# Optimization experiments

Hardware: AMD Instinct MI355X
Metric: run time of the kernel (lower is better)

Reference implementation:

```python
import jax, jax.numpy as jnp
import numpy as np

ALPHA = 0.2
BN_EPS = 1e-5
NEG = -9e15


def make_quaternion_mul(kernel):
    # kernel: [in/4, out]; split columns into quaternion components
    dim = kernel.shape[1] // 4
    r, i, j, k = jnp.split(kernel, 4, axis=1)
    r2 = jnp.concatenate([r, -i, -j, -k], axis=0)
    i2 = jnp.concatenate([i, r, -k, j], axis=0)
    j2 = jnp.concatenate([j, k, r, -i], axis=0)
    k2 = jnp.concatenate([k, -j, i, r], axis=0)
    return jnp.concatenate([r2, i2, j2, k2], axis=1)  # [in, out]


def setup_inputs() -> dict:
    key = jax.random.key(0)
    k1, k2, k3, k4 = jax.random.split(key, 4)
    N, IN, OUT = 8192, 512, 128
    inp = jax.random.normal(k1, (N, IN), dtype=jnp.float32)
    adj = jax.random.randint(k2, (N, N), 0, 2, dtype=jnp.int32)
    # xavier-like init for params
    W = jax.random.normal(k3, (IN // 4, OUT), dtype=jnp.float32) * (1.0 / np.sqrt(IN // 4))
    a = jax.random.normal(k4, (2 * OUT, 1), dtype=jnp.float32) * (1.0 / np.sqrt(2 * OUT))
    bn_gamma = jnp.ones((OUT,), dtype=jnp.float32)
    bn_beta = jnp.zeros((OUT,), dtype=jnp.float32)
    return {"input": inp, "adj": adj, "W": W, "a": a, "bn_gamma": bn_gamma, "bn_beta": bn_beta}


def reference(input, adj, W, a, bn_gamma, bn_beta):
    out_features = W.shape[1]
    hamilton = make_quaternion_mul(W)           # [in, out]
    h = input @ hamilton                        # [N, out]
    # a_input[i,j] = concat(h_i, h_j); a_input @ a decomposes as
    # (h @ a1)_i + (h @ a2)_j with a1 = a[:out], a2 = a[out:]
    a1 = a[:out_features, 0]                    # [out]
    a2 = a[out_features:, 0]                    # [out]
    s1 = h @ a1                                 # [N]
    s2 = h @ a2                                 # [N]
    e = s1[:, None] + s2[None, :]               # [N, N]
    e = jnp.where(e > 0, e, ALPHA * e)          # leaky_relu
    attention = jnp.where(adj > 0, e, NEG)
    attention = jax.nn.softmax(attention, axis=1)
    # dropout is identity in inference
    h_prime = attention @ h                     # [N, out]
    # BatchNorm1d (training-mode batch statistics, biased variance)
    mean = jnp.mean(h_prime, axis=0)
    var = jnp.var(h_prime, axis=0)
    h_prime = (h_prime - mean) / jnp.sqrt(var + BN_EPS) * bn_gamma + bn_beta
    # concat=True -> ELU
    return jax.nn.elu(h_prime)
```

## Files before the change

### kernel.cpp

```cpp
#include <hip/hip_runtime.h>
#include <hip/hip_bf16.h>
#include <math.h>

#define N_NODES 8192
#define IN_F    512
#define OUT_F   128
#define LRELU_A 0.2f
#define EPS_BN  1e-5f
#define MSH     40.0f
#define NSPLIT  8
#define JSPAN   (N_NODES / NSPLIT)
#define TILE_I  64
#define ISTR    520

typedef unsigned short u16;
typedef unsigned int   u32;
typedef unsigned long long u64;
typedef __attribute__((ext_vector_type(8))) short  short8;
typedef __attribute__((ext_vector_type(4))) float  floatx4;

__device__ __forceinline__ u16 f2bf_rtn(float x) {
    u32 u = __float_as_uint(x);
    return (u16)((u + 0x7fffu + ((u >> 16) & 1u)) >> 16);
}

__global__ __launch_bounds__(256) void k_hamT(const float* __restrict__ W, u16* __restrict__ hamF,
                                              float* __restrict__ s1, float* __restrict__ s2,
                                              float* __restrict__ cs, float* __restrict__ cq) {
    const int idx = blockIdx.x * 256 + threadIdx.x;
    if (idx < N_NODES) { s1[idx] = 0.f; s2[idx] = 0.f; }
    if (idx < OUT_F)   { cs[idx] = 0.f; cq[idx] = 0.f; }
    const int c = idx >> 9, k = idx & 511;
    const int b = c >> 5, cc = c & 31, kp = k >> 7, kq = k & 127;
    const u32 NEGMASK = 0x284Eu;
    const float sg = ((NEGMASK >> (b * 4 + kp)) & 1u) ? -1.f : 1.f;
    const int kappa = k >> 5, q = (k >> 3) & 3, e = k & 7;
    hamF[((kappa * 4 + q) * 128 + c) * 8 + e] = f2bf_rtn(sg * W[kq * 128 + (b ^ kp) * 32 + cc]);
}

__global__ __launch_bounds__(256) void k_h(const float* __restrict__ inp, const u16* __restrict__ hamF,
                                           const float* __restrict__ a,
                                           u16* __restrict__ hT, float* __restrict__ s1, float* __restrict__ s2) {
    __shared__ u16 inA[16 * ISTR];
    __shared__ float red[4][128][20];
    const int t = threadIdx.x;
    const int lane = t & 63, wid = t >> 6;
    const int quad = lane >> 4, n = lane & 15;
    const int i0 = blockIdx.x * 16;
    const int kb = wid * 128;

#pragma unroll
    for (int u = 0; u < 8; ++u) {
        float4 v = *(const float4*)&inp[(size_t)i0 * IN_F + u * 1024 + t * 4];
        const int r = u * 2 + (t >> 7);
        const int col = (t & 127) * 4;
        u64 pk = (u64)f2bf_rtn(v.x) | ((u64)f2bf_rtn(v.y) << 16)
               | ((u64)f2bf_rtn(v.z) << 32) | ((u64)f2bf_rtn(v.w) << 48);
        *(u64*)&inA[r * ISTR + col] = pk;
    }
    __syncthreads();

    floatx4 acc[8];
#pragma unroll
    for (int ct = 0; ct < 8; ++ct) acc[ct] = (floatx4){0.f, 0.f, 0.f, 0.f};

#pragma unroll
    for (int ks = 0; ks < 4; ++ks) {
        short8 fa = *(const short8*)&inA[n * ISTR + kb + ks * 32 + quad * 8];
#pragma unroll
        for (int ct = 0; ct < 8; ++ct) {
            short8 fb = *(const short8*)&hamF[((wid * 4 + ks) * 4 + quad) * 1024 + (ct * 16 + n) * 8];
            acc[ct] = __builtin_amdgcn_mfma_f32_16x16x32_bf16(fa, fb, acc[ct], 0, 0, 0);
        }
    }

    {
        float p1[4] = {0.f, 0.f, 0.f, 0.f}, p2[4] = {0.f, 0.f, 0.f, 0.f};
#pragma unroll
        for (int ct = 0; ct < 8; ++ct) {
            const int c = ct * 16 + n;
            const float a1v = a[c], a2v = a[OUT_F + c];
#pragma unroll
            for (int r = 0; r < 4; ++r) { p1[r] += acc[ct][r] * a1v; p2[r] += acc[ct][r] * a2v; }
        }
#pragma unroll
        for (int m = 1; m < 16; m <<= 1) {
#pragma unroll
            for (int r = 0; r < 4; ++r) {
                p1[r] += __shfl_xor(p1[r], m, 64);
                p2[r] += __shfl_xor(p2[r], m, 64);
            }
        }
        if (n == 0) {
#pragma unroll
            for (int r = 0; r < 4; ++r) {
                atomicAdd(&s1[i0 + quad * 4 + r], p1[r]);
                atomicAdd(&s2[i0 + quad * 4 + r], p2[r]);
            }
        }
    }

#pragma unroll
    for (int ct = 0; ct < 8; ++ct)
        *(float4*)&red[wid][ct * 16 + n][quad * 4] = *(float4*)&acc[ct];
    __syncthreads();

    {
        const int c = t >> 1, ih = (t & 1) * 8;
        float v[8];
#pragma unroll
        for (int e = 0; e < 8; ++e)
            v[e] = red[0][c][ih + e] + red[1][c][ih + e] + red[2][c][ih + e] + red[3][c][ih + e];
        uint4 pk;
        pk.x = (u32)f2bf_rtn(v[0]) | ((u32)f2bf_rtn(v[1]) << 16);
        pk.y = (u32)f2bf_rtn(v[2]) | ((u32)f2bf_rtn(v[3]) << 16);
        pk.z = (u32)f2bf_rtn(v[4]) | ((u32)f2bf_rtn(v[5]) << 16);
        pk.w = (u32)f2bf_rtn(v[6]) | ((u32)f2bf_rtn(v[7]) << 16);
        *(uint4*)&hT[(size_t)c * N_NODES + i0 + ih] = pk;
    }
}

__global__ __launch_bounds__(256, 4) void k_att(const int* __restrict__ adj, const u16* __restrict__ hT,
                                                const float* __restrict__ s1, const float* __restrict__ s2,
                                                float* __restrict__ Opart, float* __restrict__ Lpart) {
    __shared__ u16 hs[2][128 * 64];
    __shared__ float s2s[JSPAN];
    const int t = threadIdx.x;
    const int lane = t & 63, wid = t >> 6;
    const int quad = lane >> 4, n = lane & 15;
    const int i0 = blockIdx.x * TILE_I;
    const int jbase = blockIdx.y * JSPAN;
    const int i_lane = i0 + wid * 16 + n;
    const float s1v = s1[i_lane];
    const int scr = t >> 3, scj = (t & 7) * 8;

    *(float4*)&s2s[t * 4] = *(const float4*)&s2[jbase + t * 4];

    u32 M[4][8];
#pragma unroll
    for (int g = 0; g < 4; ++g)
#pragma unroll
        for (int w = 0; w < 8; ++w) M[g][w] = 0u;
    {
        const size_t rowbase = (size_t)(i0 + wid * 16);
#pragma unroll 4
        for (int rr = 0; rr < 16; ++rr) {
            const int* ap = adj + (rowbase + rr) * N_NODES + jbase + lane * 4;
            uint4 v[4];
#pragma unroll
            for (int g = 0; g < 4; ++g) v[g] = *(const uint4*)(ap + g * 256);
            const bool kp = (n == rr);
#pragma unroll
            for (int g = 0; g < 4; ++g) {
                u64 c0 = __ballot((int)v[g].x > 0);
                u64 c1 = __ballot((int)v[g].y > 0);
                u64 c2 = __ballot((int)v[g].z > 0);
                u64 c3 = __ballot((int)v[g].w > 0);
                if (kp) {
                    M[g][0] = (u32)c0; M[g][1] = (u32)(c0 >> 32);
                    M[g][2] = (u32)c1; M[g][3] = (u32)(c1 >> 32);
                    M[g][4] = (u32)c2; M[g][5] = (u32)(c2 >> 32);
                    M[g][6] = (u32)c3; M[g][7] = (u32)(c3 >> 32);
                }
            }
        }
    }

#pragma unroll
    for (int ps = 0; ps < 4; ++ps) {
        const int cr = ps * 32 + scr;
        uint4 v = *(const uint4*)&hT[(size_t)cr * N_NODES + jbase + scj];
        *(uint4*)&hs[0][cr * 64 + (scj ^ ((cr & 7) * 8))] = v;
    }
    __syncthreads();

    floatx4 acc[8];
#pragma unroll
    for (int ct = 0; ct < 8; ct++) acc[ct] = (floatx4){0.f, 0.f, 0.f, 0.f};
    float Lacc = 0.f;

#pragma unroll
    for (int g = 0; g < 4; ++g) {
#pragma unroll
        for (int chi = 0; chi < 4; ++chi) {
            const int ch = g * 4 + chi;
            const int cur = ch & 1;
            const bool more = (ch + 1 < 16);
            uint4 H[4];
            if (more) {
#pragma unroll
                for (int ps = 0; ps < 4; ++ps) {
                    const int cr = ps * 32 + scr;
                    H[ps] = *(const uint4*)&hT[(size_t)cr * N_NODES + jbase + (ch + 1) * 64 + scj];
                }
            }
            short8 fa[2];
#pragma unroll
            for (int ks = 0; ks < 2; ++ks) {
                const int jl = ch * 64 + ks * 32 + quad * 8;
                float4 sa = *(const float4*)&s2s[jl];
                float4 sb = *(const float4*)&s2s[jl + 4];
                const float sv[8] = {sa.x, sa.y, sa.z, sa.w, sb.x, sb.y, sb.z, sb.w};
                union { u32 u[4]; short8 s; } cv;
#pragma unroll
                for (int jh = 0; jh < 4; ++jh) {
                    float w2[2];
#pragma unroll
                    for (int e = 0; e < 2; ++e) {
                        const int jj = jh * 2 + e;
                        const u32 word = M[g][(jj & 3) * 2 + (chi >> 1)];
                        const int sh = (chi & 1) * 16 + ks * 8 + quad * 2 + (jj >> 2);
                        const u32 mbit = (word >> sh) & 1u;
                        float sc = s1v + sv[jj];
                        sc = fmaxf(sc, LRELU_A * sc);
                        float w = mbit ? __expf(sc - MSH) : 0.f;
                        Lacc += w;
                        w2[e] = w;
                    }
                    cv.u[jh] = (u32)f2bf_rtn(w2[0]) | ((u32)f2bf_rtn(w2[1]) << 16);
                }
                fa[ks] = cv.s;
            }
#pragma unroll
            for (int ct = 0; ct < 8; ++ct) {
                const int rb = ct * 16 + n;
                const int sw = (rb & 7) * 8;
                short8 fb0 = *(const short8*)&hs[cur][rb * 64 + ((quad * 8) ^ sw)];
                short8 fb1 = *(const short8*)&hs[cur][rb * 64 + ((32 + quad * 8) ^ sw)];
                acc[ct] = __builtin_amdgcn_mfma_f32_16x16x32_bf16(fa[0], fb0, acc[ct], 0, 0, 0);
                acc[ct] = __builtin_amdgcn_mfma_f32_16x16x32_bf16(fa[1], fb1, acc[ct], 0, 0, 0);
            }
            if (more) {
#pragma unroll
                for (int ps = 0; ps < 4; ++ps) {
                    const int cr = ps * 32 + scr;
                    *(uint4*)&hs[cur ^ 1][cr * 64 + (scj ^ ((cr & 7) * 8))] = H[ps];
                }
            }
            __syncthreads();
        }
    }

    Lacc += __shfl_xor(Lacc, 16, 64);
    Lacc += __shfl_xor(Lacc, 32, 64);
    if (lane < 16)
        Lpart[(size_t)blockIdx.y * N_NODES + i_lane] = Lacc;

    const size_t obase = (size_t)blockIdx.y * N_NODES * OUT_F;
#pragma unroll
    for (int ct = 0; ct < 8; ++ct) {
#pragma unroll
        for (int r = 0; r < 4; ++r) {
            const int i = i0 + wid * 16 + quad * 4 + r;
            Opart[obase + (size_t)i * OUT_F + ct * 16 + n] = acc[ct][r];
        }
    }
}

__global__ __launch_bounds__(256) void k_comb(const float* __restrict__ Opart, const float* __restrict__ Lpart,
                                              float* __restrict__ hp, float* __restrict__ cs, float* __restrict__ cq) {
    const int t = threadIdx.x;
    const int c = t & 127, half = t >> 7;
    const int ibase = blockIdx.x * 64;
    float sv = 0.f, sq = 0.f;
    for (int k = 0; k < 32; k++) {
        const int i = ibase + half + (k << 1);
        float o = 0.f, L = 0.f;
#pragma unroll
        for (int s = 0; s < NSPLIT; s++) {
            o += Opart[((size_t)s * N_NODES + i) * OUT_F + c];
            L += Lpart[(size_t)s * N_NODES + i];
        }
        float v = L > 0.f ? o / L : 0.f;
        hp[(size_t)i * OUT_F + c] = v;
        sv += v; sq += v * v;
    }
    __shared__ float red[256];
    red[t] = sv; __syncthreads();
    if (half == 0) atomicAdd(&cs[c], sv + red[t + 128]);
    __syncthreads(); red[t] = sq; __syncthreads();
    if (half == 0) atomicAdd(&cq[c], sq + red[t + 128]);
}

__global__ __launch_bounds__(256) void k_bn(const float* __restrict__ hp, const float* __restrict__ cs,
                                            const float* __restrict__ cq, const float* __restrict__ gamma,
                                            const float* __restrict__ beta, float* __restrict__ out) {
    const int idx = blockIdx.x * 256 + threadIdx.x;
    const int c = idx & 127;
    const float mean = cs[c] * (1.f / N_NODES);
    const float var  = cq[c] * (1.f / N_NODES) - mean * mean;
    float x = (hp[idx] - mean) * rsqrtf(var + EPS_BN) * gamma[c] + beta[c];
    x = x > 0.f ? x : expm1f(x);
    out[idx] = x;
}

extern "C" void kernel_launch(void* const* d_in, const int* in_sizes, int n_in,
                              void* d_out, int out_size, void* d_ws, size_t ws_size,
                              hipStream_t stream) {
    (void)in_sizes; (void)n_in; (void)out_size; (void)ws_size;
    const float* inp   = (const float*)d_in[0];
    const int*   adj   = (const int*)d_in[1];
    const float* W     = (const float*)d_in[2];
    const float* a     = (const float*)d_in[3];
    const float* gamma = (const float*)d_in[4];
    const float* beta  = (const float*)d_in[5];
    float* out = (float*)d_out;

    char* wsb = (char*)d_ws;
    u16*   hamF = (u16*)wsb;   wsb += (size_t)OUT_F * IN_F * 2;
    u16*   hT   = (u16*)wsb;   wsb += (size_t)OUT_F * N_NODES * 2;
    float* s1   = (float*)wsb; wsb += N_NODES * 4;
    float* s2   = (float*)wsb; wsb += N_NODES * 4;
    float* Op   = (float*)wsb; wsb += (size_t)NSPLIT * N_NODES * OUT_F * 4;
    float* Lp   = (float*)wsb; wsb += (size_t)NSPLIT * N_NODES * 4;
    float* hp   = (float*)wsb; wsb += (size_t)N_NODES * OUT_F * 4;
    float* cs   = (float*)wsb; wsb += OUT_F * 4;
    float* cq   = (float*)wsb; wsb += OUT_F * 4;

    hipLaunchKernelGGL(k_hamT, dim3(256), dim3(256), 0, stream, W, hamF, s1, s2, cs, cq);
    hipLaunchKernelGGL(k_h,    dim3(512), dim3(256), 0, stream, inp, hamF, a, hT, s1, s2);
    hipLaunchKernelGGL(k_att,  dim3(128, NSPLIT), dim3(256), 0, stream, adj, hT, s1, s2, Op, Lp);
    hipLaunchKernelGGL(k_comb, dim3(128), dim3(256), 0, stream, Op, Lp, hp, cs, cq);
    hipLaunchKernelGGL(k_bn,   dim3(4096), dim3(256), 0, stream, hp, cs, cq, gamma, beta, out);
}
```

Measured before the change: 447.3 us.

## Pipeline adjacency mask loads across attention chunks and widen combine grid

```diff
diff --git a/kernel.cpp b/kernel.cpp
--- a/kernel.cpp
+++ b/kernel.cpp
@@ -23,6 +23,19 @@
     u32 u = __float_as_uint(x);
     return (u16)((u + 0x7fffu + ((u >> 16) & 1u)) >> 16);
 }
+
+#define BALLOT4(vv, rr, MM) do {                                   \
+    u64 b0 = __ballot((int)(vv).x > 0);                            \
+    u64 b1 = __ballot((int)(vv).y > 0);                            \
+    u64 b2 = __ballot((int)(vv).z > 0);                            \
+    u64 b3 = __ballot((int)(vv).w > 0);                            \
+    if (n == (rr)) {                                               \
+        MM[0] = (u32)b0; MM[1] = (u32)(b0 >> 32);                  \
+        MM[2] = (u32)b1; MM[3] = (u32)(b1 >> 32);                  \
+        MM[4] = (u32)b2; MM[5] = (u32)(b2 >> 32);                  \
+        MM[6] = (u32)b3; MM[7] = (u32)(b3 >> 32);                  \
+    }                                                              \
+} while (0)
 
 __global__ __launch_bounds__(256) void k_hamT(const float* __restrict__ W, u16* __restrict__ hamF,
                                               float* __restrict__ s1, float* __restrict__ s2,
@@ -136,34 +149,20 @@
 
     *(float4*)&s2s[t * 4] = *(const float4*)&s2[jbase + t * 4];
 
-    u32 M[4][8];
-#pragma unroll
-    for (int g = 0; g < 4; ++g)
-#pragma unroll
-        for (int w = 0; w < 8; ++w) M[g][w] = 0u;
-    {
-        const size_t rowbase = (size_t)(i0 + wid * 16);
-#pragma unroll 4
-        for (int rr = 0; rr < 16; ++rr) {
-            const int* ap = adj + (rowbase + rr) * N_NODES + jbase + lane * 4;
-            uint4 v[4];
-#pragma unroll
-            for (int g = 0; g < 4; ++g) v[g] = *(const uint4*)(ap + g * 256);
-            const bool kp = (n == rr);
-#pragma unroll
-            for (int g = 0; g < 4; ++g) {
-                u64 c0 = __ballot((int)v[g].x > 0);
-                u64 c1 = __ballot((int)v[g].y > 0);
-                u64 c2 = __ballot((int)v[g].z > 0);
-                u64 c3 = __ballot((int)v[g].w > 0);
-                if (kp) {
-                    M[g][0] = (u32)c0; M[g][1] = (u32)(c0 >> 32);
-                    M[g][2] = (u32)c1; M[g][3] = (u32)(c1 >> 32);
-                    M[g][4] = (u32)c2; M[g][5] = (u32)(c2 >> 32);
-                    M[g][6] = (u32)c3; M[g][7] = (u32)(c3 >> 32);
-                }
-            }
-        }
+    const size_t rowbase = (size_t)(i0 + wid * 16);
+    const int* aj = adj + jbase + lane * 4;
+
+    u32 Mc[8], Mn[8];
+#pragma unroll
+    for (int w = 0; w < 8; ++w) { Mc[w] = 0u; Mn[w] = 0u; }
+#pragma unroll
+    for (int b = 0; b < 4; ++b) {
+        uint4 vv[4];
+#pragma unroll
+        for (int r = 0; r < 4; ++r)
+            vv[r] = *(const uint4*)(aj + (rowbase + b * 4 + r) * N_NODES);
+#pragma unroll
+        for (int r = 0; r < 4; ++r) BALLOT4(vv[r], b * 4 + r, Mc);
     }
 
 #pragma unroll
@@ -179,13 +178,30 @@
     for (int ct = 0; ct < 8; ct++) acc[ct] = (floatx4){0.f, 0.f, 0.f, 0.f};
     float Lacc = 0.f;
 
+    uint4 vp[4];
+
 #pragma unroll
     for (int g = 0; g < 4; ++g) {
+        if (g > 0) {
+#pragma unroll
+            for (int r = 0; r < 4; ++r) BALLOT4(vp[r], 12 + r, Mn);
+#pragma unroll
+            for (int w = 0; w < 8; ++w) Mc[w] = Mn[w];
+        }
 #pragma unroll
         for (int chi = 0; chi < 4; ++chi) {
             const int ch = g * 4 + chi;
             const int cur = ch & 1;
             const bool more = (ch + 1 < 16);
+            if (g < 3) {
+                if (chi >= 1) {
+#pragma unroll
+                    for (int r = 0; r < 4; ++r) BALLOT4(vp[r], (chi - 1) * 4 + r, Mn);
+                }
+#pragma unroll
+                for (int r = 0; r < 4; ++r)
+                    vp[r] = *(const uint4*)(aj + (rowbase + chi * 4 + r) * N_NODES + (g + 1) * 256);
+            }
             uint4 H[4];
             if (more) {
 #pragma unroll
@@ -208,7 +224,7 @@
 #pragma unroll
                     for (int e = 0; e < 2; ++e) {
                         const int jj = jh * 2 + e;
-                        const u32 word = M[g][(jj & 3) * 2 + (chi >> 1)];
+                        const u32 word = Mc[(jj & 3) * 2 + (chi >> 1)];
                         const int sh = (chi & 1) * 16 + ks * 8 + quad * 2 + (jj >> 2);
                         const u32 mbit = (word >> sh) & 1u;
                         float sc = s1v + sv[jj];
@@ -261,9 +277,9 @@
                                               float* __restrict__ hp, float* __restrict__ cs, float* __restrict__ cq) {
     const int t = threadIdx.x;
     const int c = t & 127, half = t >> 7;
-    const int ibase = blockIdx.x * 64;
+    const int ibase = blockIdx.x * 16;
     float sv = 0.f, sq = 0.f;
-    for (int k = 0; k < 32; k++) {
+    for (int k = 0; k < 8; k++) {
         const int i = ibase + half + (k << 1);
         float o = 0.f, L = 0.f;
 #pragma unroll
@@ -320,6 +336,6 @@
     hipLaunchKernelGGL(k_hamT, dim3(256), dim3(256), 0, stream, W, hamF, s1, s2, cs, cq);
     hipLaunchKernelGGL(k_h,    dim3(512), dim3(256), 0, stream, inp, hamF, a, hT, s1, s2);
     hipLaunchKernelGGL(k_att,  dim3(128, NSPLIT), dim3(256), 0, stream, adj, hT, s1, s2, Op, Lp);
-    hipLaunchKernelGGL(k_comb, dim3(128), dim3(256), 0, stream, Op, Lp, hp, cs, cq);
+    hipLaunchKernelGGL(k_comb, dim3(512), dim3(256), 0, stream, Op, Lp, hp, cs, cq);
     hipLaunchKernelGGL(k_bn,   dim3(4096), dim3(256), 0, stream, hp, cs, cq, gamma, beta, out);
 }
```

New measurement: 447.2 us. No clear change (-0.0%).
